# Performance work log

Measured on AMD Instinct MI355X. Metric: run time of the kernel, lower is better.

The kernel has to match this reference:

```python
import jax, jax.numpy as jnp
import numpy as np
from jax import lax

DN = ('NCHW', 'OIHW', 'NCHW')


def _bilinear(img, py, px):
    # img: [B,C,H,W]; py,px: [B,K2,H,W] float sampling coords (zero outside)
    B, C, H, W = img.shape
    y0 = jnp.floor(py); x0 = jnp.floor(px)
    wy1 = py - y0; wy0 = 1.0 - wy1
    wx1 = px - x0; wx0 = 1.0 - wx1

    def gather(yi, xi):
        yc = jnp.clip(yi, 0, H - 1).astype(jnp.int32)
        xc = jnp.clip(xi, 0, W - 1).astype(jnp.int32)
        valid = ((yi >= 0) & (yi <= H - 1) & (xi >= 0) & (xi <= W - 1)).astype(img.dtype)
        # per-batch advanced gather -> [B,C,K2,H,W]
        g = jax.vmap(lambda im, a, b: im[:, a, b])(img, yc, xc)
        return g * valid[:, None]

    return (gather(y0, x0) * (wy0 * wx0)[:, None]
            + gather(y0, x0 + 1) * (wy0 * wx1)[:, None]
            + gather(y0 + 1, x0) * (wy1 * wx0)[:, None]
            + gather(y0 + 1, x0 + 1) * (wy1 * wx1)[:, None])


def _deform_layer(x, ow, ob, w, b, dil=1):
    # offset conv: 3x3, stride 1, pad 1 -> [B, 18, H, W]
    B, C, H, W = x.shape
    off = lax.conv_general_dilated(x, ow, (1, 1), 'SAME', dimension_numbers=DN)
    off = off + ob[None, :, None, None]
    off = off.reshape(B, 9, 2, H, W)  # per kernel point: (dy, dx)
    oy, ox = off[:, :, 0], off[:, :, 1]
    ky, kx = jnp.meshgrid(jnp.arange(3), jnp.arange(3), indexing='ij')
    ky = ky.reshape(9).astype(x.dtype); kx = kx.reshape(9).astype(x.dtype)
    yy = jnp.arange(H, dtype=x.dtype)[:, None]
    xx = jnp.arange(W, dtype=x.dtype)[None, :]
    # sampling coords: out_pos - pad + dil*k + offset (pad == dil)
    py = yy[None, None] - dil + dil * ky[None, :, None, None] + oy
    px = xx[None, None] - dil + dil * kx[None, :, None, None] + ox
    sam = _bilinear(x, py, px)  # [B,C,9,H,W]
    out = jnp.einsum('bckhw,ock->bohw', sam, w.reshape(w.shape[0], C, 9))
    return out + b[None, :, None, None]


def setup_inputs() -> dict:
    key = jax.random.key(0)
    ks = jax.random.split(key, 5)
    L, C = 4, 256
    x = jax.random.normal(ks[0], (2, C, 96, 96), dtype=jnp.float32)
    # small offset-conv weights -> moderate offsets (torch inits them to 0)
    off_w = jax.random.normal(ks[1], (L, 18, C, 3, 3), dtype=jnp.float32) * 0.01
    off_b = jnp.zeros((L, 18), dtype=jnp.float32)
    fan_in = C * 9
    dw = jax.random.normal(ks[2], (L, C, C, 3, 3), dtype=jnp.float32) * np.sqrt(2.0 / fan_in)
    db = jnp.zeros((L, C), dtype=jnp.float32)
    return {'x': x, 'off_w': off_w, 'off_b': off_b, 'dw': dw, 'db': db}


def reference(x, off_w, off_b, dw, db):
    L = off_w.shape[0]
    for i in range(L):
        x = _deform_layer(x, off_w[i], off_b[i], dw[i], db[i], dil=1)
        x = jax.nn.relu(x)
    return x
```

## Files before the change

kernel.cpp:

```cpp
#include <hip/hip_runtime.h>

#define BN 2
#define CH 256
#define HH 96
#define WW 96
#define NL 4
#define HW (HH*WW)
#define KK (CH*9)
#define NPOS (BN*HW)

#define MPOS 32
#define NBLK (NPOS/MPOS)
#define CKCH 32
#define CKLEN (CKCH*9)
#define NCKS 4
#define SAMW2 296

#define WB_PER_L (288*256*8)
#define WB_TOT (NL*WB_PER_L)
#define OWB_PER_L (288*32*8)
#define OWB_TOT (NL*OWB_PER_L)

typedef __attribute__((ext_vector_type(8))) short short8;
typedef __attribute__((ext_vector_type(4))) float f32x4;

__device__ __forceinline__ unsigned short f2bf(float f) {
    union { float f; unsigned int u; } v; v.f = f;
    unsigned int r = v.u + 0x7fffu + ((v.u >> 16) & 1u);
    return (unsigned short)(r >> 16);
}

__global__ void prep_kernel(const float* __restrict__ dw, const float* __restrict__ off_w,
                            unsigned short* __restrict__ wB, unsigned short* __restrict__ owB) {
    int idx = blockIdx.x * 256 + threadIdx.x;
    if (idx < WB_TOT) {
        int j  = idx & 7;
        int oc = (idx >> 3) & 255;
        int g  = (idx >> 11) % 288;
        int l  = idx / WB_PER_L;
        int col = g * 8 + j;
        int ck = col / CKLEN;
        int r  = col - ck * CKLEN;
        int t9 = r >> 5;
        int ci = r & 31;
        int c  = ck * CKCH + ci;
        wB[idx] = f2bf(dw[((size_t)(l * CH + oc) * CH + c) * 9 + t9]);
    } else {
        int i2 = idx - WB_TOT;
        if (i2 >= OWB_TOT) return;
        int j   = i2 & 7;
        int ocp = (i2 >> 3) & 31;
        int g   = (i2 >> 8) % 288;
        int l   = i2 / OWB_PER_L;
        int col = g * 8 + j;
        int ck = col / CKLEN;
        int r  = col - ck * CKLEN;
        int t9 = r >> 5;
        int ci = r & 31;
        int c  = ck * CKCH + ci;
        owB[i2] = (ocp < 18) ? f2bf(off_w[((size_t)(l * 18 + ocp) * CH + c) * 9 + t9]) : 0;
    }
}

__global__ void __launch_bounds__(256)
transpose_kernel(const float* __restrict__ src, unsigned short* __restrict__ xT) {
    __shared__ float tile[64][65];
    int blk = blockIdx.x;
    int b = blk / 576, r = blk - 576 * b;
    int hw0 = (r >> 2) * 64, c0 = (r & 3) * 64;
    int tid = threadIdx.x;
    int lane = tid & 63, grp = tid >> 6;
    const float* sp = src + (size_t)(b * CH + c0) * HW + hw0;
    #pragma unroll
    for (int i = 0; i < 16; ++i) {
        int c = grp * 16 + i;
        tile[c][lane] = sp[(size_t)c * HW + lane];
    }
    __syncthreads();
    unsigned short* dp = xT + (size_t)(b * HW + hw0) * CH + c0;
    #pragma unroll
    for (int i = 0; i < 16; ++i) {
        int hw = grp * 16 + i;
        dp[(size_t)hw * CH + lane] = f2bf(tile[lane][hw]);
    }
}

__global__ void __launch_bounds__(256)
off_mfma_kernel(const unsigned short* __restrict__ xT, const unsigned short* __restrict__ owB,
                const float* __restrict__ ob, float* __restrict__ off_g) {
    __shared__ int rtab[MPOS * 9];
    const int tid = threadIdx.x;
    int pb = (int)blockIdx.x;
    pb = (pb & 7) * (NBLK / 8) + (pb >> 3);
    const int pos0 = pb * MPOS;
    const int b0   = pos0 / HW;
    const int rem0 = pos0 - b0 * HW;
    const int h0   = rem0 / WW;
    const int w0   = rem0 - h0 * WW;

    for (int rec = tid; rec < MPOS * 9; rec += 256) {
        int p = rec / 9, t9 = rec - 9 * p;
        int dy = t9 / 3 - 1, dx = t9 - 3 * (t9 / 3) - 1;
        int y = h0 + dy, xw = w0 + p + dx;
        bool valid = ((unsigned)y < HH) && ((unsigned)xw < WW);
        rtab[rec] = valid ? (y * WW + xw) * CH : -1;
    }
    __syncthreads();

    const int m   = tid & 15;
    const int q   = (tid >> 4) & 3;
    const int wvi = tid >> 6;
    const int mt  = wvi & 1;
    const int nt  = wvi >> 1;
    const int p   = mt * 16 + m;

    const unsigned short* xq = xT + (size_t)b0 * HW * CH + q * 8;
    const unsigned short* wq = owB + (size_t)(nt * 16 + m) * 8;

    f32x4 acc0 = {}, acc1 = {};
    for (int kb = 0; kb < 9; ++kb) {
        int s0 = rtab[p * 9 + kb];
        const unsigned short* ap = xq + s0;
        #pragma unroll
        for (int ck = 0; ck < 8; ++ck) {
            short8 av = {};
            if (s0 >= 0) av = *(const short8*)(ap + ck * CKCH);
            short8 bv = *(const short8*)(wq + (size_t)(ck * 36 + kb * 4 + q) * (32 * 8));
            if (ck & 1) acc1 = __builtin_amdgcn_mfma_f32_16x16x32_bf16(av, bv, acc1, 0, 0, 0);
            else        acc0 = __builtin_amdgcn_mfma_f32_16x16x32_bf16(av, bv, acc0, 0, 0, 0);
        }
    }
    int oc = nt * 16 + m;
    if (oc < 18) {
        float bsv = ob[oc];
        #pragma unroll
        for (int r = 0; r < 4; ++r) {
            int pp = mt * 16 + q * 4 + r;
            off_g[(size_t)(pos0 + pp) * 18 + oc] = acc0[r] + acc1[r] + bsv;
        }
    }
}

__global__ void __launch_bounds__(256, 5)
deform_mfma_kernel(const unsigned short* __restrict__ xT, const float* __restrict__ off_g,
                   const unsigned short* __restrict__ wB,
                   float* __restrict__ dst0, float* __restrict__ dst1) {
    __shared__ __align__(16) unsigned short sam[MPOS * SAMW2];
    __shared__ float offs[MPOS * 18];
    __shared__ __align__(16) uint4 taps4[MPOS * 9];
    __shared__ unsigned short dso16[MPOS * 9];
    const int tid = threadIdx.x;
    const int s   = (int)blockIdx.x & 1;
    int pb = (int)blockIdx.x >> 1;
    pb = (pb & 7) * (NBLK / 8) + (pb >> 3);
    const int pos0 = pb * MPOS;
    const int b0   = pos0 / HW;
    const int rem0 = pos0 - b0 * HW;
    const int h0   = rem0 / WW;
    const int w0   = rem0 - h0 * WW;

    for (int i = tid; i < MPOS * 18; i += 256)
        offs[i] = off_g[(size_t)pos0 * 18 + i];
    __syncthreads();

    for (int rec = tid; rec < MPOS * 9; rec += 256) {
        int p  = rec / 9, t9 = rec - 9 * p;
        int ky = t9 / 3, kx = t9 - 3 * (t9 / 3);
        float py = (float)(h0 - 1 + ky) + offs[p * 18 + 2 * t9];
        float px = (float)(w0 + p - 1 + kx) + offs[p * 18 + 2 * t9 + 1];
        float yf = floorf(py), xf = floorf(px);
        int y0 = (int)yf, x0 = (int)xf;
        float wy1 = py - yf, wx1 = px - xf;
        float fy0 = ((unsigned)y0       < HH) ? 1.f - wy1 : 0.f;
        float fy1 = ((unsigned)(y0 + 1) < HH) ? wy1       : 0.f;
        float fx0 = ((unsigned)x0       < WW) ? 1.f - wx1 : 0.f;
        float fx1 = ((unsigned)(x0 + 1) < WW) ? wx1       : 0.f;
        int y0c = min(max(y0, 0), HH - 1), y1c = min(max(y0 + 1, 0), HH - 1);
        int x0c = min(max(x0, 0), WW - 1), x1c = min(max(x0 + 1, 0), WW - 1);
        int bx  = min(max(x0, 0), WW - 2);
        float wA  = (x0c == bx     ? fx0 : 0.f) + (x1c == bx     ? fx1 : 0.f);
        float wBv = (x0c == bx + 1 ? fx0 : 0.f) + (x1c == bx + 1 ? fx1 : 0.f);
        uint4 tv;
        tv.x = (unsigned int)((y0c * WW + bx) * CH);
        tv.y = (unsigned int)((y1c * WW + bx) * CH);
        tv.z = (unsigned int)f2bf(fy0 * wA) | ((unsigned int)f2bf(fy0 * wBv) << 16);
        tv.w = (unsigned int)f2bf(fy1 * wA) | ((unsigned int)f2bf(fy1 * wBv) << 16);
        taps4[rec] = tv;
        dso16[rec] = (unsigned short)(p * SAMW2 + t9 * 32);
    }

    const int lane = tid & 63;
    const int wvi  = tid >> 6;
    const int cp   = lane & 15;
    const int rsub = lane >> 4;
    const int m    = tid & 15;
    const int q    = (tid >> 4) & 3;

    f32x4 acc[2][4] = {};
    const unsigned short* xTb = xT + (size_t)b0 * HW * CH;

    for (int ckl = 0; ckl < NCKS; ++ckl) {
        const int ck = s * NCKS + ckl;
        __syncthreads();
        const unsigned short* xs = xTb + ck * CKCH + cp * 2;
        #pragma unroll 3
        for (int rr = 0; rr < 18; ++rr) {
            int rec = wvi * 72 + rr * 4 + rsub;
            uint4 tv = taps4[rec];
            int dso  = dso16[rec];
            float u0 = __uint_as_float(tv.z << 16);
            float u1 = __uint_as_float(tv.z & 0xFFFF0000u);
            float u2 = __uint_as_float(tv.w << 16);
            float u3 = __uint_as_float(tv.w & 0xFFFF0000u);
            unsigned int A0, A1, C0, C1;
            __builtin_memcpy(&A0, xs + tv.x, 4);
            __builtin_memcpy(&A1, xs + tv.x + CH, 4);
            __builtin_memcpy(&C0, xs + tv.y, 4);
            __builtin_memcpy(&C1, xs + tv.y + CH, 4);
            float2 a0 = make_float2(__uint_as_float(A0 << 16), __uint_as_float(A0 & 0xFFFF0000u));
            float2 a1 = make_float2(__uint_as_float(A1 << 16), __uint_as_float(A1 & 0xFFFF0000u));
            float2 c0 = make_float2(__uint_as_float(C0 << 16), __uint_as_float(C0 & 0xFFFF0000u));
            float2 c1 = make_float2(__uint_as_float(C1 << 16), __uint_as_float(C1 & 0xFFFF0000u));
            float2 vv;
            vv.x = a0.x * u0;               vv.y = a0.y * u0;
            vv.x = fmaf(a1.x, u1, vv.x);    vv.y = fmaf(a1.y, u1, vv.y);
            vv.x = fmaf(c0.x, u2, vv.x);    vv.y = fmaf(c0.y, u2, vv.y);
            vv.x = fmaf(c1.x, u3, vv.x);    vv.y = fmaf(c1.y, u3, vv.y);
            unsigned int packed = (unsigned int)f2bf(vv.x) | ((unsigned int)f2bf(vv.y) << 16);
            *(unsigned int*)(sam + dso + cp * 2) = packed;
        }
        __syncthreads();
        const unsigned short* arow0 = sam + m * SAMW2 + q * 8;
        const unsigned short* arow1 = arow0 + 16 * SAMW2;
        const int g0 = ck * 36;
        for (int kb = 0; kb < 9; ++kb) {
            short8 av0 = *(const short8*)(arow0 + kb * 32);
            short8 av1 = *(const short8*)(arow1 + kb * 32);
            const unsigned short* wkb = wB + ((size_t)(g0 + kb * 4 + q) * 256
                                             + (wvi * 64 + m)) * 8;
            #pragma unroll
            for (int t = 0; t < 4; ++t) {
                short8 bv = *(const short8*)(wkb + t * 16 * 8);
                acc[0][t] = __builtin_amdgcn_mfma_f32_16x16x32_bf16(av0, bv, acc[0][t], 0, 0, 0);
                acc[1][t] = __builtin_amdgcn_mfma_f32_16x16x32_bf16(av1, bv, acc[1][t], 0, 0, 0);
            }
        }
    }

    float* dst = s ? dst1 : dst0;
    float* cT = (float*)sam;
    #pragma unroll
    for (int mt = 0; mt < 2; ++mt) {
        __syncthreads();
        #pragma unroll
        for (int t = 0; t < 4; ++t) {
            int oc = wvi * 64 + t * 16 + m;
            #pragma unroll
            for (int r = 0; r < 4; ++r)
                cT[oc * 17 + q * 4 + r] = acc[mt][t][r];
        }
        __syncthreads();
        float* dp = dst + (size_t)(pos0 + mt * 16) * CH + tid;
        #pragma unroll 4
        for (int p = 0; p < 16; ++p)
            dp[(size_t)p * CH] = cT[tid * 17 + p];
    }
}

__global__ void __launch_bounds__(256)
sum_cl_kernel(const float* __restrict__ p0, const float* __restrict__ p1,
              const float* __restrict__ db, unsigned short* __restrict__ xT) {
    unsigned int idx = blockIdx.x * 256 + threadIdx.x;
    unsigned int e = idx * 4;
    unsigned int oc = e & (CH - 1);
    float4 bsv = *(const float4*)(db + oc);
    float4 a = *(const float4*)(p0 + e);
    float4 b = *(const float4*)(p1 + e);
    unsigned short o[4];
    o[0] = f2bf(fmaxf(a.x + b.x + bsv.x, 0.f));
    o[1] = f2bf(fmaxf(a.y + b.y + bsv.y, 0.f));
    o[2] = f2bf(fmaxf(a.z + b.z + bsv.z, 0.f));
    o[3] = f2bf(fmaxf(a.w + b.w + bsv.w, 0.f));
    __builtin_memcpy(xT + e, o, 8);
}

__global__ void __launch_bounds__(256)
sum_nchw_kernel(const float* __restrict__ p0, const float* __restrict__ p1,
                const float* __restrict__ db, float* __restrict__ out) {
    __shared__ float tile[64][65];
    int blk = blockIdx.x;
    int hw0 = (blk >> 2) * 64;
    int oc0 = (blk & 3) * 64;
    int tid = threadIdx.x;
    int lane = tid & 63, grp = tid >> 6;
    float bsv = db[oc0 + lane];
    #pragma unroll
    for (int i = 0; i < 16; ++i) {
        int r = grp * 16 + i;
        size_t e = (size_t)(hw0 + r) * CH + oc0 + lane;
        tile[r][lane] = fmaxf(p0[e] + p1[e] + bsv, 0.f);
    }
    __syncthreads();
    int b = hw0 / HW, hwl = hw0 - b * HW;
    #pragma unroll
    for (int i = 0; i < 16; ++i) {
        int oc = grp * 16 + i;
        out[((size_t)(b * CH) + oc0 + oc) * HW + hwl + lane] = tile[lane][oc];
    }
}

extern "C" void kernel_launch(void* const* d_in, const int* in_sizes, int n_in,
                              void* d_out, int out_size, void* d_ws, size_t ws_size,
                              hipStream_t stream) {
    const float* x     = (const float*)d_in[0];
    const float* off_w = (const float*)d_in[1];
    const float* off_b = (const float*)d_in[2];
    const float* dw    = (const float*)d_in[3];
    const float* db    = (const float*)d_in[4];

    float* ws   = (float*)d_ws;
    float* p0    = ws;
    float* p1    = p0 + (size_t)NPOS * CH;
    float* off_g = p1 + (size_t)NPOS * CH;
    unsigned short* wB  = (unsigned short*)(off_g + (size_t)NPOS * 18);
    unsigned short* owB = wB + WB_TOT;
    unsigned short* xT  = owB + OWB_TOT;

    prep_kernel<<<(WB_TOT + OWB_TOT + 255) / 256, 256, 0, stream>>>(dw, off_w, wB, owB);
    transpose_kernel<<<BN * 576, 256, 0, stream>>>(x, xT);

    for (int l = 0; l < NL; ++l) {
        off_mfma_kernel<<<NBLK, 256, 0, stream>>>(
            xT, owB + (size_t)l * OWB_PER_L, off_b + l * 18, off_g);
        deform_mfma_kernel<<<NBLK * 2, 256, 0, stream>>>(
            xT, off_g, wB + (size_t)l * WB_PER_L, p0, p1);
        if (l < NL - 1)
            sum_cl_kernel<<<(NPOS * CH / 4) / 256, 256, 0, stream>>>(p0, p1, db + l * CH, xT);
        else
            sum_nchw_kernel<<<(NPOS / 64) * 4, 256, 0, stream>>>(p0, p1, db + l * CH,
                                                                 (float*)d_out);
    }
}
```

Baseline: 434.7 us.

## Fuse offset conv, deformable conv, and bias/ReLU epilogue into one per-layer kernel

Replaces the per-layer sequence of offset-conv, deform-conv (split over two channel halves writing fp32 partials), and sum/ReLU kernels with a single 512-thread kernel per layer. The offset conv is computed in-block with K split across wave halves and reduced through shared memory. Each block then handles all 256 input channels, so no fp32 partial buffers are needed, and bias+ReLU+bf16 store (or the final NCHW store) is done in the epilogue. Activations ping-pong between two bf16 buffers. This removes launches and the global round trips of partials and offsets, but it halves the grid size and raises per-block shared-memory and register pressure, which may reduce occupancy.

```diff
diff --git a/kernel.cpp b/kernel.cpp
--- a/kernel.cpp
+++ b/kernel.cpp
@@ -13,7 +13,6 @@
 #define NBLK (NPOS/MPOS)
 #define CKCH 32
 #define CKLEN (CKCH*9)
-#define NCKS 4
 #define SAMW2 296
 
 #define WB_PER_L (288*256*8)
@@ -85,9 +84,15 @@
     }
 }
 
-__global__ void __launch_bounds__(256)
-off_mfma_kernel(const unsigned short* __restrict__ xT, const unsigned short* __restrict__ owB,
-                const float* __restrict__ ob, float* __restrict__ off_g) {
+__global__ void __launch_bounds__(512)
+layer_kernel(const unsigned short* __restrict__ xT, const unsigned short* __restrict__ owB,
+             const float* __restrict__ ob, const unsigned short* __restrict__ wB,
+             const float* __restrict__ db, unsigned short* __restrict__ xTo,
+             float* __restrict__ outF, int last) {
+    __shared__ __align__(16) unsigned short sam[MPOS * SAMW2];
+    __shared__ float offs[MPOS * 18];
+    __shared__ __align__(16) uint4 taps4[MPOS * 9];
+    __shared__ unsigned short dso16[MPOS * 9];
     __shared__ int rtab[MPOS * 9];
     const int tid = threadIdx.x;
     int pb = (int)blockIdx.x;
@@ -98,7 +103,7 @@
     const int h0   = rem0 / WW;
     const int w0   = rem0 - h0 * WW;
 
-    for (int rec = tid; rec < MPOS * 9; rec += 256) {
+    for (int rec = tid; rec < MPOS * 9; rec += 512) {
         int p = rec / 9, t9 = rec - 9 * p;
         int dy = t9 / 3 - 1, dx = t9 - 3 * (t9 / 3) - 1;
         int y = h0 + dy, xw = w0 + p + dx;
@@ -110,60 +115,47 @@
     const int m   = tid & 15;
     const int q   = (tid >> 4) & 3;
     const int wvi = tid >> 6;
-    const int mt  = wvi & 1;
-    const int nt  = wvi >> 1;
-    const int p   = mt * 16 + m;
-
-    const unsigned short* xq = xT + (size_t)b0 * HW * CH + q * 8;
-    const unsigned short* wq = owB + (size_t)(nt * 16 + m) * 8;
-
-    f32x4 acc0 = {}, acc1 = {};
-    for (int kb = 0; kb < 9; ++kb) {
-        int s0 = rtab[p * 9 + kb];
-        const unsigned short* ap = xq + s0;
-        #pragma unroll
-        for (int ck = 0; ck < 8; ++ck) {
-            short8 av = {};
-            if (s0 >= 0) av = *(const short8*)(ap + ck * CKCH);
-            short8 bv = *(const short8*)(wq + (size_t)(ck * 36 + kb * 4 + q) * (32 * 8));
-            if (ck & 1) acc1 = __builtin_amdgcn_mfma_f32_16x16x32_bf16(av, bv, acc1, 0, 0, 0);
-            else        acc0 = __builtin_amdgcn_mfma_f32_16x16x32_bf16(av, bv, acc0, 0, 0, 0);
-        }
-    }
-    int oc = nt * 16 + m;
-    if (oc < 18) {
-        float bsv = ob[oc];
-        #pragma unroll
-        for (int r = 0; r < 4; ++r) {
-            int pp = mt * 16 + q * 4 + r;
-            off_g[(size_t)(pos0 + pp) * 18 + oc] = acc0[r] + acc1[r] + bsv;
-        }
-    }
-}
-
-__global__ void __launch_bounds__(256, 5)
-deform_mfma_kernel(const unsigned short* __restrict__ xT, const float* __restrict__ off_g,
-                   const unsigned short* __restrict__ wB,
-                   float* __restrict__ dst0, float* __restrict__ dst1) {
-    __shared__ __align__(16) unsigned short sam[MPOS * SAMW2];
-    __shared__ float offs[MPOS * 18];
-    __shared__ __align__(16) uint4 taps4[MPOS * 9];
-    __shared__ unsigned short dso16[MPOS * 9];
-    const int tid = threadIdx.x;
-    const int s   = (int)blockIdx.x & 1;
-    int pb = (int)blockIdx.x >> 1;
-    pb = (pb & 7) * (NBLK / 8) + (pb >> 3);
-    const int pos0 = pb * MPOS;
-    const int b0   = pos0 / HW;
-    const int rem0 = pos0 - b0 * HW;
-    const int h0   = rem0 / WW;
-    const int w0   = rem0 - h0 * WW;
-
-    for (int i = tid; i < MPOS * 18; i += 256)
-        offs[i] = off_g[(size_t)pos0 * 18 + i];
+
+    {
+        const int mt  = wvi & 1;
+        const int ntq = (wvi >> 1) & 1;
+        const int kh  = wvi >> 2;
+        const int p   = mt * 16 + m;
+        const unsigned short* xq = xT + (size_t)b0 * HW * CH + q * 8;
+        const unsigned short* wq = owB + (size_t)(ntq * 16 + m) * 8;
+        f32x4 a0 = {}, a1 = {};
+        for (int kb = 0; kb < 9; ++kb) {
+            int s0 = rtab[p * 9 + kb];
+            const unsigned short* ap = xq + s0;
+            #pragma unroll
+            for (int ckl = 0; ckl < 4; ++ckl) {
+                int ck = kh * 4 + ckl;
+                short8 av = {};
+                if (s0 >= 0) av = *(const short8*)(ap + ck * CKCH);
+                short8 bv = *(const short8*)(wq + (size_t)(ck * 36 + kb * 4 + q) * (32 * 8));
+                if (ckl & 1) a1 = __builtin_amdgcn_mfma_f32_16x16x32_bf16(av, bv, a1, 0, 0, 0);
+                else         a0 = __builtin_amdgcn_mfma_f32_16x16x32_bf16(av, bv, a0, 0, 0, 0);
+            }
+        }
+        float* offp = (float*)sam;
+        int oc = ntq * 16 + m;
+        if (oc < 18) {
+            #pragma unroll
+            for (int r = 0; r < 4; ++r) {
+                int pp = mt * 16 + q * 4 + r;
+                offp[(kh * 32 + pp) * 20 + oc] = a0[r] + a1[r];
+            }
+        }
+    }
     __syncthreads();
-
-    for (int rec = tid; rec < MPOS * 9; rec += 256) {
+    for (int i = tid; i < MPOS * 18; i += 512) {
+        int p = i / 18, oc = i - 18 * p;
+        const float* offp = (const float*)sam;
+        offs[i] = offp[p * 20 + oc] + offp[(32 + p) * 20 + oc] + ob[oc];
+    }
+    __syncthreads();
+
+    for (int rec = tid; rec < MPOS * 9; rec += 512) {
         int p  = rec / 9, t9 = rec - 9 * p;
         int ky = t9 / 3, kx = t9 - 3 * (t9 / 3);
         float py = (float)(h0 - 1 + ky) + offs[p * 18 + 2 * t9];
@@ -189,23 +181,20 @@
         dso16[rec] = (unsigned short)(p * SAMW2 + t9 * 32);
     }
 
-    const int lane = tid & 63;
-    const int wvi  = tid >> 6;
-    const int cp   = lane & 15;
-    const int rsub = lane >> 4;
-    const int m    = tid & 15;
-    const int q    = (tid >> 4) & 3;
-
-    f32x4 acc[2][4] = {};
+    const int g   = tid >> 4;
+    const int cp  = tid & 15;
+    const int mtg = wvi & 1;
+    const int ntg = wvi >> 1;
+
+    f32x4 acc[4] = {};
     const unsigned short* xTb = xT + (size_t)b0 * HW * CH;
 
-    for (int ckl = 0; ckl < NCKS; ++ckl) {
-        const int ck = s * NCKS + ckl;
+    for (int ck = 0; ck < 8; ++ck) {
         __syncthreads();
         const unsigned short* xs = xTb + ck * CKCH + cp * 2;
         #pragma unroll 3
-        for (int rr = 0; rr < 18; ++rr) {
-            int rec = wvi * 72 + rr * 4 + rsub;
+        for (int it = 0; it < 9; ++it) {
+            int rec = it * 32 + g;
             uint4 tv = taps4[rec];
             int dso  = dso16[rec];
             float u0 = __uint_as_float(tv.z << 16);
@@ -230,82 +219,58 @@
             *(unsigned int*)(sam + dso + cp * 2) = packed;
         }
         __syncthreads();
-        const unsigned short* arow0 = sam + m * SAMW2 + q * 8;
-        const unsigned short* arow1 = arow0 + 16 * SAMW2;
+        const unsigned short* arow = sam + (mtg * 16 + m) * SAMW2 + q * 8;
         const int g0 = ck * 36;
         for (int kb = 0; kb < 9; ++kb) {
-            short8 av0 = *(const short8*)(arow0 + kb * 32);
-            short8 av1 = *(const short8*)(arow1 + kb * 32);
+            short8 av = *(const short8*)(arow + kb * 32);
             const unsigned short* wkb = wB + ((size_t)(g0 + kb * 4 + q) * 256
-                                             + (wvi * 64 + m)) * 8;
+                                             + (ntg * 64 + m)) * 8;
             #pragma unroll
             for (int t = 0; t < 4; ++t) {
                 short8 bv = *(const short8*)(wkb + t * 16 * 8);
-                acc[0][t] = __builtin_amdgcn_mfma_f32_16x16x32_bf16(av0, bv, acc[0][t], 0, 0, 0);
-                acc[1][t] = __builtin_amdgcn_mfma_f32_16x16x32_bf16(av1, bv, acc[1][t], 0, 0, 0);
-            }
-        }
-    }
-
-    float* dst = s ? dst1 : dst0;
+                acc[t] = __builtin_amdgcn_mfma_f32_16x16x32_bf16(av, bv, acc[t], 0, 0, 0);
+            }
+        }
+    }
+
     float* cT = (float*)sam;
     #pragma unroll
-    for (int mt = 0; mt < 2; ++mt) {
+    for (int pass = 0; pass < 2; ++pass) {
         __syncthreads();
-        #pragma unroll
-        for (int t = 0; t < 4; ++t) {
-            int oc = wvi * 64 + t * 16 + m;
-            #pragma unroll
-            for (int r = 0; r < 4; ++r)
-                cT[oc * 17 + q * 4 + r] = acc[mt][t][r];
+        if (mtg == pass) {
+            #pragma unroll
+            for (int t = 0; t < 4; ++t) {
+                int oc = ntg * 64 + t * 16 + m;
+                #pragma unroll
+                for (int r = 0; r < 4; ++r)
+                    cT[oc * 17 + q * 4 + r] = acc[t][r];
+            }
         }
         __syncthreads();
-        float* dp = dst + (size_t)(pos0 + mt * 16) * CH + tid;
-        #pragma unroll 4
-        for (int p = 0; p < 16; ++p)
-            dp[(size_t)p * CH] = cT[tid * 17 + p];
-    }
-}
-
-__global__ void __launch_bounds__(256)
-sum_cl_kernel(const float* __restrict__ p0, const float* __restrict__ p1,
-              const float* __restrict__ db, unsigned short* __restrict__ xT) {
-    unsigned int idx = blockIdx.x * 256 + threadIdx.x;
-    unsigned int e = idx * 4;
-    unsigned int oc = e & (CH - 1);
-    float4 bsv = *(const float4*)(db + oc);
-    float4 a = *(const float4*)(p0 + e);
-    float4 b = *(const float4*)(p1 + e);
-    unsigned short o[4];
-    o[0] = f2bf(fmaxf(a.x + b.x + bsv.x, 0.f));
-    o[1] = f2bf(fmaxf(a.y + b.y + bsv.y, 0.f));
-    o[2] = f2bf(fmaxf(a.z + b.z + bsv.z, 0.f));
-    o[3] = f2bf(fmaxf(a.w + b.w + bsv.w, 0.f));
-    __builtin_memcpy(xT + e, o, 8);
-}
-
-__global__ void __launch_bounds__(256)
-sum_nchw_kernel(const float* __restrict__ p0, const float* __restrict__ p1,
-                const float* __restrict__ db, float* __restrict__ out) {
-    __shared__ float tile[64][65];
-    int blk = blockIdx.x;
-    int hw0 = (blk >> 2) * 64;
-    int oc0 = (blk & 3) * 64;
-    int tid = threadIdx.x;
-    int lane = tid & 63, grp = tid >> 6;
-    float bsv = db[oc0 + lane];
-    #pragma unroll
-    for (int i = 0; i < 16; ++i) {
-        int r = grp * 16 + i;
-        size_t e = (size_t)(hw0 + r) * CH + oc0 + lane;
-        tile[r][lane] = fmaxf(p0[e] + p1[e] + bsv, 0.f);
-    }
-    __syncthreads();
-    int b = hw0 / HW, hwl = hw0 - b * HW;
-    #pragma unroll
-    for (int i = 0; i < 16; ++i) {
-        int oc = grp * 16 + i;
-        out[((size_t)(b * CH) + oc0 + oc) * HW + hwl + lane] = tile[lane][oc];
+        if (!last) {
+            int oc2 = (tid & 127) * 2;
+            int pb4 = (tid >> 7) * 4;
+            float bv0 = db[oc2], bv1 = db[oc2 + 1];
+            unsigned short* dp = xTo + (size_t)(pos0 + pass * 16) * CH + oc2;
+            #pragma unroll
+            for (int j = 0; j < 4; ++j) {
+                int p = pb4 + j;
+                float v0 = fmaxf(cT[oc2 * 17 + p] + bv0, 0.f);
+                float v1 = fmaxf(cT[(oc2 + 1) * 17 + p] + bv1, 0.f);
+                unsigned int pk = (unsigned int)f2bf(v0) | ((unsigned int)f2bf(v1) << 16);
+                *(unsigned int*)(dp + (size_t)p * CH) = pk;
+            }
+        } else {
+            const int lane = tid & 63;
+            const int po = lane & 15;
+            const int os = lane >> 4;
+            #pragma unroll
+            for (int it = 0; it < 8; ++it) {
+                int oc = wvi * 32 + it * 4 + os;
+                float v = fmaxf(cT[oc * 17 + po] + db[oc], 0.f);
+                outF[((size_t)(b0 * CH) + oc) * HW + rem0 + pass * 16 + po] = v;
+            }
+        }
     }
 }
 
@@ -318,26 +283,20 @@
     const float* dw    = (const float*)d_in[3];
     const float* db    = (const float*)d_in[4];
 
-    float* ws   = (float*)d_ws;
-    float* p0    = ws;
-    float* p1    = p0 + (size_t)NPOS * CH;
-    float* off_g = p1 + (size_t)NPOS * CH;
-    unsigned short* wB  = (unsigned short*)(off_g + (size_t)NPOS * 18);
+    unsigned short* xT0 = (unsigned short*)d_ws;
+    unsigned short* xT1 = xT0 + (size_t)NPOS * CH;
+    unsigned short* wB  = xT1 + (size_t)NPOS * CH;
     unsigned short* owB = wB + WB_TOT;
-    unsigned short* xT  = owB + OWB_TOT;
 
     prep_kernel<<<(WB_TOT + OWB_TOT + 255) / 256, 256, 0, stream>>>(dw, off_w, wB, owB);
-    transpose_kernel<<<BN * 576, 256, 0, stream>>>(x, xT);
+    transpose_kernel<<<BN * 576, 256, 0, stream>>>(x, xT0);
 
     for (int l = 0; l < NL; ++l) {
-        off_mfma_kernel<<<NBLK, 256, 0, stream>>>(
-            xT, owB + (size_t)l * OWB_PER_L, off_b + l * 18, off_g);
-        deform_mfma_kernel<<<NBLK * 2, 256, 0, stream>>>(
-            xT, off_g, wB + (size_t)l * WB_PER_L, p0, p1);
-        if (l < NL - 1)
-            sum_cl_kernel<<<(NPOS * CH / 4) / 256, 256, 0, stream>>>(p0, p1, db + l * CH, xT);
-        else
-            sum_nchw_kernel<<<(NPOS / 64) * 4, 256, 0, stream>>>(p0, p1, db + l * CH,
-                                                                 (float*)d_out);
-    }
-}
+        unsigned short* cur = (l & 1) ? xT1 : xT0;
+        unsigned short* nxt = (l & 1) ? xT0 : xT1;
+        layer_kernel<<<NBLK, 512, 0, stream>>>(
+            cur, owB + (size_t)l * OWB_PER_L, off_b + l * 18,
+            wB + (size_t)l * WB_PER_L, db + l * CH,
+            nxt, (float*)d_out, (l == NL - 1) ? 1 : 0);
+    }
+}
```

Result: slower. 534.2 us (+22.9%).

## Fuse offset convolution into deformable conv kernel, dropping separate offset pass

Applied to the files above, without the earlier changes.

Computes the 3x3 offset convolution via MFMA inside each deform block and writes offsets directly to shared memory, removing the separate offset kernel launch and its global offset buffer round trip. Because each position tile is handled by two blocks (channel halves), the offset conv is now computed redundantly twice per tile, and the deform kernel gains extra shared memory and register pressure under its occupancy bound.

```diff
diff --git a/kernel.cpp b/kernel.cpp
--- a/kernel.cpp
+++ b/kernel.cpp
@@ -85,70 +85,15 @@
     }
 }
 
-__global__ void __launch_bounds__(256)
-off_mfma_kernel(const unsigned short* __restrict__ xT, const unsigned short* __restrict__ owB,
-                const float* __restrict__ ob, float* __restrict__ off_g) {
-    __shared__ int rtab[MPOS * 9];
-    const int tid = threadIdx.x;
-    int pb = (int)blockIdx.x;
-    pb = (pb & 7) * (NBLK / 8) + (pb >> 3);
-    const int pos0 = pb * MPOS;
-    const int b0   = pos0 / HW;
-    const int rem0 = pos0 - b0 * HW;
-    const int h0   = rem0 / WW;
-    const int w0   = rem0 - h0 * WW;
-
-    for (int rec = tid; rec < MPOS * 9; rec += 256) {
-        int p = rec / 9, t9 = rec - 9 * p;
-        int dy = t9 / 3 - 1, dx = t9 - 3 * (t9 / 3) - 1;
-        int y = h0 + dy, xw = w0 + p + dx;
-        bool valid = ((unsigned)y < HH) && ((unsigned)xw < WW);
-        rtab[rec] = valid ? (y * WW + xw) * CH : -1;
-    }
-    __syncthreads();
-
-    const int m   = tid & 15;
-    const int q   = (tid >> 4) & 3;
-    const int wvi = tid >> 6;
-    const int mt  = wvi & 1;
-    const int nt  = wvi >> 1;
-    const int p   = mt * 16 + m;
-
-    const unsigned short* xq = xT + (size_t)b0 * HW * CH + q * 8;
-    const unsigned short* wq = owB + (size_t)(nt * 16 + m) * 8;
-
-    f32x4 acc0 = {}, acc1 = {};
-    for (int kb = 0; kb < 9; ++kb) {
-        int s0 = rtab[p * 9 + kb];
-        const unsigned short* ap = xq + s0;
-        #pragma unroll
-        for (int ck = 0; ck < 8; ++ck) {
-            short8 av = {};
-            if (s0 >= 0) av = *(const short8*)(ap + ck * CKCH);
-            short8 bv = *(const short8*)(wq + (size_t)(ck * 36 + kb * 4 + q) * (32 * 8));
-            if (ck & 1) acc1 = __builtin_amdgcn_mfma_f32_16x16x32_bf16(av, bv, acc1, 0, 0, 0);
-            else        acc0 = __builtin_amdgcn_mfma_f32_16x16x32_bf16(av, bv, acc0, 0, 0, 0);
-        }
-    }
-    int oc = nt * 16 + m;
-    if (oc < 18) {
-        float bsv = ob[oc];
-        #pragma unroll
-        for (int r = 0; r < 4; ++r) {
-            int pp = mt * 16 + q * 4 + r;
-            off_g[(size_t)(pos0 + pp) * 18 + oc] = acc0[r] + acc1[r] + bsv;
-        }
-    }
-}
-
 __global__ void __launch_bounds__(256, 5)
-deform_mfma_kernel(const unsigned short* __restrict__ xT, const float* __restrict__ off_g,
-                   const unsigned short* __restrict__ wB,
+deform_mfma_kernel(const unsigned short* __restrict__ xT, const unsigned short* __restrict__ owB,
+                   const float* __restrict__ ob, const unsigned short* __restrict__ wB,
                    float* __restrict__ dst0, float* __restrict__ dst1) {
     __shared__ __align__(16) unsigned short sam[MPOS * SAMW2];
     __shared__ float offs[MPOS * 18];
     __shared__ __align__(16) uint4 taps4[MPOS * 9];
     __shared__ unsigned short dso16[MPOS * 9];
+    __shared__ int rtab[MPOS * 9];
     const int tid = threadIdx.x;
     const int s   = (int)blockIdx.x & 1;
     int pb = (int)blockIdx.x >> 1;
@@ -159,8 +104,48 @@
     const int h0   = rem0 / WW;
     const int w0   = rem0 - h0 * WW;
 
-    for (int i = tid; i < MPOS * 18; i += 256)
-        offs[i] = off_g[(size_t)pos0 * 18 + i];
+    for (int rec = tid; rec < MPOS * 9; rec += 256) {
+        int p = rec / 9, t9 = rec - 9 * p;
+        int dy = t9 / 3 - 1, dx = t9 - 3 * (t9 / 3) - 1;
+        int y = h0 + dy, xw = w0 + p + dx;
+        bool valid = ((unsigned)y < HH) && ((unsigned)xw < WW);
+        rtab[rec] = valid ? (y * WW + xw) * CH : -1;
+    }
+    __syncthreads();
+
+    const int m   = tid & 15;
+    const int q   = (tid >> 4) & 3;
+    const int wvi = tid >> 6;
+
+    {
+        const int mt  = wvi & 1;
+        const int ntq = wvi >> 1;
+        const int p   = mt * 16 + m;
+        const unsigned short* xq = xT + (size_t)b0 * HW * CH + q * 8;
+        const unsigned short* wq = owB + (size_t)(ntq * 16 + m) * 8;
+        f32x4 a0 = {}, a1 = {};
+        for (int kb = 0; kb < 9; ++kb) {
+            int s0 = rtab[p * 9 + kb];
+            const unsigned short* ap = xq + s0;
+            #pragma unroll
+            for (int ck = 0; ck < 8; ++ck) {
+                short8 av = {};
+                if (s0 >= 0) av = *(const short8*)(ap + ck * CKCH);
+                short8 bv = *(const short8*)(wq + (size_t)(ck * 36 + kb * 4 + q) * (32 * 8));
+                if (ck & 1) a1 = __builtin_amdgcn_mfma_f32_16x16x32_bf16(av, bv, a1, 0, 0, 0);
+                else        a0 = __builtin_amdgcn_mfma_f32_16x16x32_bf16(av, bv, a0, 0, 0, 0);
+            }
+        }
+        int oc = ntq * 16 + m;
+        if (oc < 18) {
+            float bsv = ob[oc];
+            #pragma unroll
+            for (int r = 0; r < 4; ++r) {
+                int pp = mt * 16 + q * 4 + r;
+                offs[pp * 18 + oc] = a0[r] + a1[r] + bsv;
+            }
+        }
+    }
     __syncthreads();
 
     for (int rec = tid; rec < MPOS * 9; rec += 256) {
@@ -190,11 +175,8 @@
     }
 
     const int lane = tid & 63;
-    const int wvi  = tid >> 6;
     const int cp   = lane & 15;
     const int rsub = lane >> 4;
-    const int m    = tid & 15;
-    const int q    = (tid >> 4) & 3;
 
     f32x4 acc[2][4] = {};
     const unsigned short* xTb = xT + (size_t)b0 * HW * CH;
@@ -321,8 +303,7 @@
     float* ws   = (float*)d_ws;
     float* p0    = ws;
     float* p1    = p0 + (size_t)NPOS * CH;
-    float* off_g = p1 + (size_t)NPOS * CH;
-    unsigned short* wB  = (unsigned short*)(off_g + (size_t)NPOS * 18);
+    unsigned short* wB  = (unsigned short*)(p1 + (size_t)NPOS * CH);
     unsigned short* owB = wB + WB_TOT;
     unsigned short* xT  = owB + OWB_TOT;
 
@@ -330,10 +311,9 @@
     transpose_kernel<<<BN * 576, 256, 0, stream>>>(x, xT);
 
     for (int l = 0; l < NL; ++l) {
-        off_mfma_kernel<<<NBLK, 256, 0, stream>>>(
-            xT, owB + (size_t)l * OWB_PER_L, off_b + l * 18, off_g);
         deform_mfma_kernel<<<NBLK * 2, 256, 0, stream>>>(
-            xT, off_g, wB + (size_t)l * WB_PER_L, p0, p1);
+            xT, owB + (size_t)l * OWB_PER_L, off_b + l * 18,
+            wB + (size_t)l * WB_PER_L, p0, p1);
         if (l < NL - 1)
             sum_cl_kernel<<<(NPOS * CH / 4) / 256, 256, 0, stream>>>(p0, p1, db + l * CH, xT);
         else
```

After: 488.0 us. 1.12x slower.

## Split offset conv over channel chunks into four partial sums reduced in deform kernel

Applied to the files above, without the earlier changes.

The offset-convolution kernel is split-K across four channel slices, so the grid grows from NBLK to 4*NBLK blocks, each doing a quarter of the MFMA work. Partial results go to four separate buffers with a padded stride of 20. The deform kernel sums the four partials and adds the offset bias when it loads the offsets. This raises parallelism and occupancy for a small kernel that had few blocks, at the cost of more global writes and reads of partial sums and a larger workspace.

```diff
diff --git a/kernel.cpp b/kernel.cpp
--- a/kernel.cpp
+++ b/kernel.cpp
@@ -87,10 +87,11 @@
 
 __global__ void __launch_bounds__(256)
 off_mfma_kernel(const unsigned short* __restrict__ xT, const unsigned short* __restrict__ owB,
-                const float* __restrict__ ob, float* __restrict__ off_g) {
+                float* __restrict__ off_p) {
     __shared__ int rtab[MPOS * 9];
     const int tid = threadIdx.x;
-    int pb = (int)blockIdx.x;
+    const int sp  = (int)blockIdx.x & 3;
+    int pb = (int)blockIdx.x >> 2;
     pb = (pb & 7) * (NBLK / 8) + (pb >> 3);
     const int pos0 = pb * MPOS;
     const int b0   = pos0 / HW;
@@ -122,28 +123,29 @@
         int s0 = rtab[p * 9 + kb];
         const unsigned short* ap = xq + s0;
         #pragma unroll
-        for (int ck = 0; ck < 8; ++ck) {
+        for (int ckl = 0; ckl < 2; ++ckl) {
+            int ck = sp * 2 + ckl;
             short8 av = {};
             if (s0 >= 0) av = *(const short8*)(ap + ck * CKCH);
             short8 bv = *(const short8*)(wq + (size_t)(ck * 36 + kb * 4 + q) * (32 * 8));
-            if (ck & 1) acc1 = __builtin_amdgcn_mfma_f32_16x16x32_bf16(av, bv, acc1, 0, 0, 0);
-            else        acc0 = __builtin_amdgcn_mfma_f32_16x16x32_bf16(av, bv, acc0, 0, 0, 0);
+            if (ckl & 1) acc1 = __builtin_amdgcn_mfma_f32_16x16x32_bf16(av, bv, acc1, 0, 0, 0);
+            else         acc0 = __builtin_amdgcn_mfma_f32_16x16x32_bf16(av, bv, acc0, 0, 0, 0);
         }
     }
     int oc = nt * 16 + m;
     if (oc < 18) {
-        float bsv = ob[oc];
+        float* op = off_p + (size_t)sp * NPOS * 20 + oc;
         #pragma unroll
         for (int r = 0; r < 4; ++r) {
             int pp = mt * 16 + q * 4 + r;
-            off_g[(size_t)(pos0 + pp) * 18 + oc] = acc0[r] + acc1[r] + bsv;
+            op[(size_t)(pos0 + pp) * 20] = acc0[r] + acc1[r];
         }
     }
 }
 
 __global__ void __launch_bounds__(256, 5)
-deform_mfma_kernel(const unsigned short* __restrict__ xT, const float* __restrict__ off_g,
-                   const unsigned short* __restrict__ wB,
+deform_mfma_kernel(const unsigned short* __restrict__ xT, const float* __restrict__ off_p,
+                   const float* __restrict__ ob, const unsigned short* __restrict__ wB,
                    float* __restrict__ dst0, float* __restrict__ dst1) {
     __shared__ __align__(16) unsigned short sam[MPOS * SAMW2];
     __shared__ float offs[MPOS * 18];
@@ -159,8 +161,12 @@
     const int h0   = rem0 / WW;
     const int w0   = rem0 - h0 * WW;
 
-    for (int i = tid; i < MPOS * 18; i += 256)
-        offs[i] = off_g[(size_t)pos0 * 18 + i];
+    for (int i = tid; i < MPOS * 18; i += 256) {
+        int p = i / 18, oc = i - 18 * p;
+        const float* bp = off_p + (size_t)(pos0 + p) * 20 + oc;
+        offs[i] = bp[0] + bp[(size_t)NPOS * 20] + bp[(size_t)NPOS * 40]
+                + bp[(size_t)NPOS * 60] + ob[oc];
+    }
     __syncthreads();
 
     for (int rec = tid; rec < MPOS * 9; rec += 256) {
@@ -321,8 +327,8 @@
     float* ws   = (float*)d_ws;
     float* p0    = ws;
     float* p1    = p0 + (size_t)NPOS * CH;
-    float* off_g = p1 + (size_t)NPOS * CH;
-    unsigned short* wB  = (unsigned short*)(off_g + (size_t)NPOS * 18);
+    float* off_p = p1 + (size_t)NPOS * CH;
+    unsigned short* wB  = (unsigned short*)(off_p + (size_t)4 * NPOS * 20);
     unsigned short* owB = wB + WB_TOT;
     unsigned short* xT  = owB + OWB_TOT;
 
@@ -330,10 +336,10 @@
     transpose_kernel<<<BN * 576, 256, 0, stream>>>(x, xT);
 
     for (int l = 0; l < NL; ++l) {
-        off_mfma_kernel<<<NBLK, 256, 0, stream>>>(
-            xT, owB + (size_t)l * OWB_PER_L, off_b + l * 18, off_g);
+        off_mfma_kernel<<<NBLK * 4, 256, 0, stream>>>(
+            xT, owB + (size_t)l * OWB_PER_L, off_p);
         deform_mfma_kernel<<<NBLK * 2, 256, 0, stream>>>(
-            xT, off_g, wB + (size_t)l * WB_PER_L, p0, p1);
+            xT, off_p, off_b + l * 18, wB + (size_t)l * WB_PER_L, p0, p1);
         if (l < NL - 1)
             sum_cl_kernel<<<(NPOS * CH / 4) / 256, 256, 0, stream>>>(p0, p1, db + l * CH, xT);
         else
```

New measurement: 433.2 us. About the same (-0.3%).
